# Performance work log

Hardware: AMD Instinct MI355X
Metric: run time of the kernel (lower is better)

The kernel has to match this reference:

```python
import jax, jax.numpy as jnp
import numpy as np

NUM_SEGMENTS = 128  # number of graphs (index.max()+1)


def setup_inputs() -> dict:
    key = jax.random.key(0)
    k1, k2, k3 = jax.random.split(key, 3)
    N, F, T, S, B = 200000, 3, 32, 32, NUM_SEGMENTS
    x = jax.random.normal(k1, (N, F), dtype=jnp.float32)
    v = jax.random.normal(k2, (F, T), dtype=jnp.float32)
    # lin exactly as in the module: linspace(-r, r, bump_steps).view(-1,1,1)
    lin = jnp.linspace(-1.1, 1.1, S, dtype=jnp.float32).reshape(S, 1, 1)
    index = jnp.sort(jax.random.randint(k3, (N,), 0, B, dtype=jnp.int64))
    return {"x": x, "index": index, "v": v, "lin": lin, "scale": 500}


def reference(x, index, v, lin, scale):
    # nh: node heights [N, T]
    nh = x @ v
    # ecc: [S, N, T] broadcasted sigmoid bump
    ecc = jax.nn.sigmoid(scale * (lin - nh))
    # scatter-add over nodes into per-graph bins, then movedim(0,1):
    # segment_sum over leading axis after transposing to [N, S, T]
    # gives [B, S, T] directly (== index_add over dim 1 then movedim).
    out = jax.ops.segment_sum(jnp.transpose(ecc, (1, 0, 2)), index,
                              num_segments=NUM_SEGMENTS)
    return out
```

## Files before the change

kernel.cpp:

```cpp
#include <hip/hip_runtime.h>

#define NSEG 128
#define SSTEPS 32
#define TDIM 32
#define NG 8
#define DROWS 37
#define SPB 8
#define CSTR (DROWS * TDIM)
#define UNR 4

__global__ __launch_bounds__(256) void ect_kernel(
    const float* __restrict__ x,
    const int*   __restrict__ idx,
    const float* __restrict__ v,
    const float* __restrict__ lin,
    const int*   __restrict__ scale_p,
    float*       __restrict__ out,
    int N)
{
    __shared__ float d[NG][DROWS][TDIM];
    __shared__ int s_bounds[2];

    const int tid = threadIdx.x;
    const unsigned bx = blockIdx.x;
    const int b = bx >> 3;
    const int j = bx & (SPB - 1);

    if (tid < 64) {
        const int L = tid & 31;
        const int h = tid >> 5;
        const int target = b + h;
        const int g0 = (int)(((long long)target * N) >> 7);

        const int hi_last = idx[N - 1];
        int p1 = g0 - 1024 + 64 * L;
        int pc1 = min(max(p1, 0), N - 1);
        int val32 = idx[pc1];
        const bool is64 = (hi_last == 0);
        int val = is64 ? idx[2 * pc1] : val32;

        bool pred1 = (p1 < 0) ? true : ((p1 >= N) ? false : (val < target));
        unsigned long long m1 = __ballot(pred1);
        unsigned hm1 = (unsigned)(m1 >> (h * 32));

        if (hm1 == 0u || hm1 == 0xFFFFFFFFu) {
            if (L == 0) {
                int lo = 0, hi = N;
                while (lo < hi) {
                    int mid = (lo + hi) >> 1;
                    int vv = is64 ? idx[2 * mid] : idx[mid];
                    if (vv < target) lo = mid + 1; else hi = mid;
                }
                s_bounds[h] = lo;
            }
        } else {
            const int A = g0 - 1024 + 64 * (31 - __builtin_clz(hm1));
            int p2 = A + 1 + 2 * L;
            int pc2 = min(max(p2, 0), N - 1);
            int v2 = is64 ? idx[2 * pc2] : idx[pc2];
            bool pred2 = (p2 < 0) ? true : ((p2 >= N) ? false : (v2 < target));
            unsigned long long m2 = __ballot(pred2);
            unsigned hm2 = (unsigned)(m2 >> (h * 32));
            const int B = hm2 ? (A + 1 + 2 * (31 - __builtin_clz(hm2))) : A;
            int p3 = B + 1;
            int pc3 = min(p3, N - 1);
            int v3 = is64 ? idx[2 * pc3] : idx[pc3];
            bool pred3 = (p3 >= N) ? false : (v3 < target);
            if (L == 0) s_bounds[h] = pred3 ? (B + 2) : (B + 1);
        }
    }
    {
        float4* dz = (float4*)d;
        for (int i = tid; i < NG * CSTR / 4; i += 256)
            dz[i] = make_float4(0.f, 0.f, 0.f, 0.f);
    }

    const float lin0 = lin[0];
    const float step = lin[1] - lin0;
    const float inv_step = 1.0f / step;
    const float negl0 = -lin0 * inv_step;
    const float scale = (float)scale_p[0];
    const float zstep = scale * step;
    const float C = __expf(zstep);

    const int t = tid & 31;
    const int g = tid >> 5;
    const float v0 = v[t], v1 = v[TDIM + t], v2 = v[2 * TDIM + t];
    float* dg = &d[g][0][t];

    __syncthreads();

    const int start = s_bounds[0], end = s_bounds[1];
    const int cnt = end - start;
    const int chunk = (cnt + SPB - 1) / SPB;
    const int k0 = start + j * chunk;
    const int k1 = min(k0 + chunk, end);

    auto process = [&](float x0, float x1, float x2) {
        const float nh = fmaf(x0, v0, fmaf(x1, v1, x2 * v2));

        float u = fmaf(nh, inv_step, negl0);
        u = fminf(fmaxf(u, -2.0f), 34.0f);
        const float sf = floorf(u);
        const int s_lo = (int)sf;

        const float E = __expf((sf - u) * zstep);
        const float rc = __builtin_amdgcn_rcpf(1.0f + E);
        const float sig0  = E * rc;
        const float sig1c = __builtin_amdgcn_rcpf(fmaf(E, C, 1.0f));

        float w0 = sig0;
        float w1 = 1.0f - sig0 - sig1c;
        float w2 = sig1c;

        if (s_lo < 0) {
            if (s_lo == -1) { w0 = w0 + w1; w1 = w2; w2 = 0.f; }
            else            { w0 = 1.0f;    w1 = 0.f; w2 = 0.f; }
        }
        const int base = max(s_lo, 0);

        float* p = dg + base * 32;
        const float a0 = p[0];
        const float a1 = p[32];
        const float a2 = p[64];
        p[0]  = a0 + w0;
        p[32] = a1 + w1;
        p[64] = a2 + w2;
    };

    {
        int k = k0 + g;
        const int nit = (k < k1) ? ((k1 - k) + NG - 1) / NG : 0;
        const int nb = nit / UNR;

        float cx[UNR][3];
        if (nb > 0) {
            #pragma unroll
            for (int i = 0; i < UNR; ++i) {
                const int kk = k + i * NG;
                cx[i][0] = x[kk * 3 + 0];
                cx[i][1] = x[kk * 3 + 1];
                cx[i][2] = x[kk * 3 + 2];
            }
        }
        for (int bi = 0; bi < nb; ++bi) {
            const int knext = k + UNR * NG;
            const bool more = (bi + 1 < nb);
            float nx[UNR][3];
            #pragma unroll
            for (int i = 0; i < UNR; ++i) {
                const int kk = more ? (knext + i * NG) : k;
                nx[i][0] = x[kk * 3 + 0];
                nx[i][1] = x[kk * 3 + 1];
                nx[i][2] = x[kk * 3 + 2];
            }
            #pragma unroll
            for (int i = 0; i < UNR; ++i)
                process(cx[i][0], cx[i][1], cx[i][2]);
            #pragma unroll
            for (int i = 0; i < UNR; ++i) {
                cx[i][0] = nx[i][0]; cx[i][1] = nx[i][1]; cx[i][2] = nx[i][2];
            }
            k = knext;
        }
        for (k = k0 + g + nb * UNR * NG; k < k1; k += NG)
            process(x[k * 3 + 0], x[k * 3 + 1], x[k * 3 + 2]);
    }
    __syncthreads();

    {
        const float* basep = (const float*)d;
        float4 sum = make_float4(0.f, 0.f, 0.f, 0.f);
        #pragma unroll
        for (int gg = 0; gg < NG; ++gg) {
            const float4 vq = ((const float4*)(basep + gg * CSTR))[tid];
            sum.x += vq.x; sum.y += vq.y; sum.z += vq.z; sum.w += vq.w;
        }
        ((float4*)d)[tid] = sum;
    }
    __syncthreads();

    if (tid < TDIM) {
        float* df = (float*)d;
        float run = 0.f;
        #pragma unroll
        for (int s = 0; s < SSTEPS; ++s) {
            run += df[s * 32 + tid];
            df[s * 32 + tid] = run;
        }
    }
    __syncthreads();

    {
        const float* df = (const float*)d;
        float* ob = out + (size_t)b * (SSTEPS * TDIM);
        #pragma unroll
        for (int q = 0; q < 4; ++q)
            atomicAdd(&ob[q * 256 + tid], df[q * 256 + tid]);
    }
}

extern "C" void kernel_launch(void* const* d_in, const int* in_sizes, int n_in,
                              void* d_out, int out_size, void* d_ws, size_t ws_size,
                              hipStream_t stream) {
    const float* x     = (const float*)d_in[0];
    const int*   index = (const int*)d_in[1];
    const float* v     = (const float*)d_in[2];
    const float* lin   = (const float*)d_in[3];
    const int*   scale = (const int*)d_in[4];
    float* out = (float*)d_out;
    const int N = in_sizes[0] / 3;

    hipMemsetAsync(d_out, 0, (size_t)out_size * sizeof(float), stream);
    ect_kernel<<<NSEG * SPB, 256, 0, stream>>>(x, index, v, lin, scale, out, N);
}
```

Measured before the change: 73.29 us.

## Share LDS histogram copies via atomics to shrink LDS and double blocks

Cuts the per-block LDS histogram from eight warp-private copies to two shared copies, with the four warps that share a copy using LDS atomicAdd instead of plain read-modify-write. It pads the histogram by two rows so negative bins need no branches, then folds those rows into the prefix scan. Blocks per segment go from 8 to 16, unrolling drops to 2, and launch bounds request 8 blocks per CU, all to raise occupancy and parallelism. The trade-off is LDS atomic contention between warps and twice as many global atomic adds per segment.

```diff
diff --git a/kernel.cpp b/kernel.cpp
--- a/kernel.cpp
+++ b/kernel.cpp
@@ -3,13 +3,13 @@
 #define NSEG 128
 #define SSTEPS 32
 #define TDIM 32
-#define NG 8
-#define DROWS 37
-#define SPB 8
+#define NGC 2
+#define DROWS 39
+#define SPB 16
 #define CSTR (DROWS * TDIM)
-#define UNR 4
-
-__global__ __launch_bounds__(256) void ect_kernel(
+#define UNR 2
+
+__global__ __launch_bounds__(256, 8) void ect_kernel(
     const float* __restrict__ x,
     const int*   __restrict__ idx,
     const float* __restrict__ v,
@@ -18,12 +18,12 @@
     float*       __restrict__ out,
     int N)
 {
-    __shared__ float d[NG][DROWS][TDIM];
+    __shared__ float d[NGC][DROWS][TDIM];
     __shared__ int s_bounds[2];
 
     const int tid = threadIdx.x;
     const unsigned bx = blockIdx.x;
-    const int b = bx >> 3;
+    const int b = bx >> 4;
     const int j = bx & (SPB - 1);
 
     if (tid < 64) {
@@ -71,7 +71,7 @@
     }
     {
         float4* dz = (float4*)d;
-        for (int i = tid; i < NG * CSTR / 4; i += 256)
+        for (int i = tid; i < NGC * CSTR / 4; i += 256)
             dz[i] = make_float4(0.f, 0.f, 0.f, 0.f);
     }
 
@@ -86,7 +86,7 @@
     const int t = tid & 31;
     const int g = tid >> 5;
     const float v0 = v[t], v1 = v[TDIM + t], v2 = v[2 * TDIM + t];
-    float* dg = &d[g][0][t];
+    float* dg = &d[g & 1][0][t];
 
     __syncthreads();
 
@@ -95,6 +95,7 @@
     const int chunk = (cnt + SPB - 1) / SPB;
     const int k0 = start + j * chunk;
     const int k1 = min(k0 + chunk, end);
+    const int NGRP = 8;
 
     auto process = [&](float x0, float x1, float x2) {
         const float nh = fmaf(x0, v0, fmaf(x1, v1, x2 * v2));
@@ -102,54 +103,45 @@
         float u = fmaf(nh, inv_step, negl0);
         u = fminf(fmaxf(u, -2.0f), 34.0f);
         const float sf = floorf(u);
-        const int s_lo = (int)sf;
+        const int base = (int)sf + 2;
 
         const float E = __expf((sf - u) * zstep);
         const float rc = __builtin_amdgcn_rcpf(1.0f + E);
         const float sig0  = E * rc;
         const float sig1c = __builtin_amdgcn_rcpf(fmaf(E, C, 1.0f));
 
-        float w0 = sig0;
-        float w1 = 1.0f - sig0 - sig1c;
-        float w2 = sig1c;
-
-        if (s_lo < 0) {
-            if (s_lo == -1) { w0 = w0 + w1; w1 = w2; w2 = 0.f; }
-            else            { w0 = 1.0f;    w1 = 0.f; w2 = 0.f; }
-        }
-        const int base = max(s_lo, 0);
+        const float w0 = sig0;
+        const float w1 = 1.0f - sig0 - sig1c;
+        const float w2 = sig1c;
 
         float* p = dg + base * 32;
-        const float a0 = p[0];
-        const float a1 = p[32];
-        const float a2 = p[64];
-        p[0]  = a0 + w0;
-        p[32] = a1 + w1;
-        p[64] = a2 + w2;
+        atomicAdd(&p[0],  w0);
+        atomicAdd(&p[32], w1);
+        atomicAdd(&p[64], w2);
     };
 
     {
         int k = k0 + g;
-        const int nit = (k < k1) ? ((k1 - k) + NG - 1) / NG : 0;
+        const int nit = (k < k1) ? ((k1 - k) + NGRP - 1) / NGRP : 0;
         const int nb = nit / UNR;
 
         float cx[UNR][3];
         if (nb > 0) {
             #pragma unroll
             for (int i = 0; i < UNR; ++i) {
-                const int kk = k + i * NG;
+                const int kk = k + i * NGRP;
                 cx[i][0] = x[kk * 3 + 0];
                 cx[i][1] = x[kk * 3 + 1];
                 cx[i][2] = x[kk * 3 + 2];
             }
         }
         for (int bi = 0; bi < nb; ++bi) {
-            const int knext = k + UNR * NG;
+            const int knext = k + UNR * NGRP;
             const bool more = (bi + 1 < nb);
             float nx[UNR][3];
             #pragma unroll
             for (int i = 0; i < UNR; ++i) {
-                const int kk = more ? (knext + i * NG) : k;
+                const int kk = more ? (knext + i * NGRP) : k;
                 nx[i][0] = x[kk * 3 + 0];
                 nx[i][1] = x[kk * 3 + 1];
                 nx[i][2] = x[kk * 3 + 2];
@@ -163,30 +155,29 @@
             }
             k = knext;
         }
-        for (k = k0 + g + nb * UNR * NG; k < k1; k += NG)
+        for (k = k0 + g + nb * UNR * NGRP; k < k1; k += NGRP)
             process(x[k * 3 + 0], x[k * 3 + 1], x[k * 3 + 2]);
     }
     __syncthreads();
 
     {
-        const float* basep = (const float*)d;
-        float4 sum = make_float4(0.f, 0.f, 0.f, 0.f);
-        #pragma unroll
-        for (int gg = 0; gg < NG; ++gg) {
-            const float4 vq = ((const float4*)(basep + gg * CSTR))[tid];
-            sum.x += vq.x; sum.y += vq.y; sum.z += vq.z; sum.w += vq.w;
-        }
-        ((float4*)d)[tid] = sum;
+        float4* c0 = (float4*)d;
+        const float4* c1 = (const float4*)((const float*)d + CSTR);
+        for (int i = tid; i < CSTR / 4; i += 256) {
+            float4 a = c0[i]; const float4 bq = c1[i];
+            a.x += bq.x; a.y += bq.y; a.z += bq.z; a.w += bq.w;
+            c0[i] = a;
+        }
     }
     __syncthreads();
 
     if (tid < TDIM) {
         float* df = (float*)d;
-        float run = 0.f;
+        float run = df[tid] + df[32 + tid];
         #pragma unroll
         for (int s = 0; s < SSTEPS; ++s) {
-            run += df[s * 32 + tid];
-            df[s * 32 + tid] = run;
+            run += df[(s + 2) * 32 + tid];
+            df[(s + 2) * 32 + tid] = run;
         }
     }
     __syncthreads();
@@ -196,7 +187,7 @@
         float* ob = out + (size_t)b * (SSTEPS * TDIM);
         #pragma unroll
         for (int q = 0; q < 4; ++q)
-            atomicAdd(&ob[q * 256 + tid], df[q * 256 + tid]);
+            atomicAdd(&ob[q * 256 + tid], df[64 + q * 256 + tid]);
     }
 }
 
```

Measured after the change: 162.9 us. 2.22x slower.
